# Kernel optimization log

Hardware: AMD Instinct MI355X
Metric: run time of the kernel (lower is better)

## Reference

```python
import jax, jax.numpy as jnp
import numpy as np

H_DIM = 64      # input_dim of edge_aggregation (== h_dim)
HID = 128       # hidden_size of each per-edge-type agg MLP
T = 5           # edge_types for non-nba dataset
B, E, N = 64, 1024, 512


def setup_inputs() -> dict:
    key = jax.random.key(0)
    ks = jax.random.split(key, 8)
    edge_distribution = jax.random.uniform(ks[0], (B, E, T), dtype=jnp.float32)
    H = jax.random.uniform(ks[1], (B, E, N), dtype=jnp.float32)
    ori = jax.random.normal(ks[2], (B, N, H_DIM), dtype=jnp.float32)
    s1 = 1.0 / np.sqrt(H_DIM)
    s2 = 1.0 / np.sqrt(HID)
    # stacked per-edge-type MLP params: Linear(64->128) -> ReLU -> Linear(128->64)
    W1 = jax.random.uniform(ks[3], (T, H_DIM, HID), minval=-s1, maxval=s1, dtype=jnp.float32)
    b1 = jax.random.uniform(ks[4], (T, HID), minval=-s1, maxval=s1, dtype=jnp.float32)
    W2 = jax.random.uniform(ks[5], (T, HID, H_DIM), minval=-s2, maxval=s2, dtype=jnp.float32)
    b2 = jax.random.uniform(ks[6], (T, H_DIM), minval=-s2, maxval=s2, dtype=jnp.float32)
    return {"edge_distribution": edge_distribution, "H": H, "ori": ori,
            "W1": W1, "b1": b1, "W2": W2, "b2": b2}


def reference(edge_distribution, H, ori, W1, b1, W2, b2):
    # incidence gather: hyperedge features [B, E, D]
    edges = jnp.matmul(H, ori)
    # per-edge-type 2-layer MLP, vectorized over the T edge types
    h = jax.nn.relu(jnp.einsum('bed,tdh->bteh', edges, W1) + b1[None, :, None, :])
    per_type = jnp.einsum('bteh,thd->bted', h, W2) + b2[None, :, None, :]
    # mixture-weighted sum over edge types -> [B, E, D]
    edge_feature = jnp.einsum('bet,bted->bed', edge_distribution, per_type)
    # scatter back through H^T and concat with original node features
    node_agg = jnp.einsum('ben,bed->bnd', H, edge_feature)  # H^T @ edge_feature
    node_feature = jnp.concatenate((node_agg, ori), axis=-1)  # [B, N, 2D]
    return node_feature
```

## Files before the change

### kernel.cpp

```cpp
#include <hip/hip_runtime.h>

#define B_   64
#define E_   1024
#define N_   512
#define D_   64
#define HID_ 128
#define T_   5

typedef __bf16 bf16x8 __attribute__((ext_vector_type(8)));
typedef float f32x4 __attribute__((ext_vector_type(4)));

__device__ __forceinline__ unsigned short f2bu(float f) {
    union { float f; unsigned int u; } v; v.f = f;
    unsigned int r = (v.u + 0x7fffu + ((v.u >> 16) & 1u)) >> 16;
    return (unsigned short)r;
}

__device__ __forceinline__ unsigned int pack2(float lo, float hi) {
    union { __bf16 b[2]; unsigned int u; } v;
    v.b[0] = (__bf16)lo; v.b[1] = (__bf16)hi;
    return v.u;
}

__device__ __forceinline__ uint4 cvt8(float4 a, float4 b) {
    union { __bf16 h[8]; uint4 u; } v;
    v.h[0] = (__bf16)a.x; v.h[1] = (__bf16)a.y; v.h[2] = (__bf16)a.z; v.h[3] = (__bf16)a.w;
    v.h[4] = (__bf16)b.x; v.h[5] = (__bf16)b.y; v.h[6] = (__bf16)b.z; v.h[7] = (__bf16)b.w;
    return v.u;
}

#define MFMA16(a, b, c) __builtin_amdgcn_mfma_f32_16x16x32_bf16((a), (b), (c), 0, 0, 0)

__global__ __launch_bounds__(256) void k_prep_w(const float* __restrict__ W1,
                                                const float* __restrict__ W2,
                                                unsigned short* __restrict__ W1T,
                                                unsigned short* __restrict__ W2T) {
    int idx = blockIdx.x * 256 + threadIdx.x;
    if (idx < T_ * HID_ * D_) {
        int t = idx / (HID_ * D_), rem = idx % (HID_ * D_);
        int h = rem / D_, d = rem % D_;
        W1T[idx] = f2bu(W1[(t * D_ + d) * HID_ + h]);
    } else {
        int j = idx - T_ * HID_ * D_;
        int t = j / (D_ * HID_), rem = j % (D_ * HID_);
        int d = rem / HID_, h = rem % HID_;
        W2T[j] = f2bu(W2[(t * HID_ + h) * D_ + d]);
    }
}

__global__ __launch_bounds__(256) void k_ori_prep(const float* __restrict__ ori,
                                                  float* __restrict__ out,
                                                  unsigned short* __restrict__ oriT) {
    int b = blockIdx.y, n0 = blockIdx.x * 64;
    __shared__ float tl[64 * 65];
    int tid = threadIdx.x;
    int dl = tid & 63;
    #pragma unroll 4
    for (int p = 0; p < 16; ++p) {
        int nn = p * 4 + (tid >> 6);
        float v = ori[(size_t)(b * N_ + n0 + nn) * D_ + dl];
        out[(size_t)(b * N_ + n0 + nn) * 128 + 64 + dl] = v;
        tl[dl * 65 + nn] = v;
    }
    __syncthreads();
    #pragma unroll 4
    for (int p = 0; p < 16; ++p) {
        int dd = p * 4 + (tid >> 6);
        oriT[(size_t)(b * D_ + dd) * N_ + n0 + dl] = f2bu(tl[dd * 65 + dl]);
    }
}

__global__ __launch_bounds__(256) void k_edge_mlp(const float* __restrict__ H,
                                                  const unsigned short* __restrict__ oriT,
                                                  const float* __restrict__ ed,
                                                  const float* __restrict__ b1,
                                                  const float* __restrict__ b2,
                                                  const unsigned short* __restrict__ W1T,
                                                  const unsigned short* __restrict__ W2T,
                                                  unsigned short* __restrict__ efT) {
    int bx = blockIdx.x;
    int b = bx >> 4, e0 = (bx & 15) * 64;
    __shared__ __align__(16) unsigned short X[17920];
    __shared__ __align__(16) unsigned short a_sh[64 * 72];
    __shared__ __align__(16) unsigned short h_sh[64 * 136];
    __shared__ float wd_sh[320];
    __shared__ float b1_sh[640];
    __shared__ float b2_sh[320];
    int tid = threadIdx.x, w = tid >> 6, l = tid & 63, q = l >> 4, c = l & 15;

    for (int u = tid; u < 320; u += 256) wd_sh[u] = ed[((size_t)b * E_ + e0) * T_ + u];
    for (int u = tid; u < 640; u += 256) b1_sh[u] = b1[u];
    for (int u = tid; u < 320; u += 256) b2_sh[u] = b2[u];

    const f32x4 zero = {0.f, 0.f, 0.f, 0.f};

    unsigned short* aA = X;
    unsigned short* bB = X + 4608;
    f32x4 acc1[4];
    #pragma unroll
    for (int fn = 0; fn < 4; ++fn) acc1[fn] = zero;

    for (int ks = 0; ks < 8; ++ks) {
        int k0 = ks * 64;
        #pragma unroll
        for (int p = 0; p < 2; ++p) {
            int u = p * 256 + tid, r = u >> 3, sg = u & 7;
            const float* s = &H[((size_t)b * E_ + e0 + r) * N_ + k0 + sg * 8];
            float4 f0 = *(const float4*)&s[0];
            float4 f1 = *(const float4*)&s[4];
            *(uint4*)&aA[r * 72 + sg * 8] = cvt8(f0, f1);
        }
        #pragma unroll
        for (int p = 0; p < 2; ++p) {
            int u = p * 256 + tid, r = u >> 3, sg = u & 7;
            *(uint4*)&bB[r * 72 + sg * 8] =
                *(const uint4*)&oriT[((size_t)b * D_ + r) * N_ + k0 + sg * 8];
        }
        __syncthreads();
        #pragma unroll
        for (int h = 0; h < 2; ++h) {
            bf16x8 a0 = *(const bf16x8*)&aA[(w * 16 + c) * 72 + h * 32 + q * 8];
            #pragma unroll
            for (int fn = 0; fn < 4; ++fn) {
                bf16x8 bb = *(const bf16x8*)&bB[(fn * 16 + c) * 72 + h * 32 + q * 8];
                acc1[fn] = MFMA16(a0, bb, acc1[fn]);
            }
        }
        __syncthreads();
    }

    #pragma unroll
    for (int fn = 0; fn < 4; ++fn)
        #pragma unroll
        for (int i = 0; i < 4; ++i)
            a_sh[(w * 16 + q * 4 + i) * 72 + fn * 16 + c] = f2bu(acc1[fn][i]);

    bf16x8 afr[2];
    #pragma unroll
    for (int ks = 0; ks < 2; ++ks)
        afr[ks] = *(const bf16x8*)&a_sh[(w * 16 + c) * 72 + ks * 32 + q * 8];

    unsigned short* w1_sh = X;
    unsigned short* w2_sh = X + 9216;

    f32x4 y[4];
    #pragma unroll
    for (int fn = 0; fn < 4; ++fn) y[fn] = zero;

    for (int t = 0; t < T_; ++t) {
        #pragma unroll
        for (int p = 0; p < 4; ++p) {
            int u2 = p * 256 + tid, hh = u2 >> 3, sg = u2 & 7;
            *(uint4*)&w1_sh[hh * 72 + sg * 8] =
                *(const uint4*)&W1T[((size_t)t * HID_ + hh) * D_ + sg * 8];
        }
        #pragma unroll
        for (int p = 0; p < 4; ++p) {
            int u2 = p * 256 + tid, dd = u2 >> 4, sg = u2 & 15;
            *(uint4*)&w2_sh[dd * 136 + sg * 8] =
                *(const uint4*)&W2T[((size_t)t * D_ + dd) * HID_ + sg * 8];
        }
        __syncthreads();

        f32x4 hc[8];
        #pragma unroll
        for (int fn = 0; fn < 8; ++fn) hc[fn] = zero;
        #pragma unroll
        for (int ks = 0; ks < 2; ++ks) {
            #pragma unroll
            for (int fn = 0; fn < 8; ++fn) {
                bf16x8 bb = *(const bf16x8*)&w1_sh[(fn * 16 + c) * 72 + ks * 32 + q * 8];
                hc[fn] = MFMA16(afr[ks], bb, hc[fn]);
            }
        }
        float wv[4];
        #pragma unroll
        for (int i = 0; i < 4; ++i) wv[i] = wd_sh[(w * 16 + q * 4 + i) * T_ + t];
        #pragma unroll
        for (int fn = 0; fn < 8; ++fn) {
            float b1v = b1_sh[t * HID_ + fn * 16 + c];
            #pragma unroll
            for (int i = 0; i < 4; ++i) {
                float v = hc[fn][i] + b1v;
                v = fmaxf(v, 0.0f) * wv[i];
                h_sh[(w * 16 + q * 4 + i) * 136 + fn * 16 + c] = f2bu(v);
            }
        }
        #pragma unroll
        for (int ks = 0; ks < 4; ++ks) {
            bf16x8 a = *(const bf16x8*)&h_sh[(w * 16 + c) * 136 + ks * 32 + q * 8];
            #pragma unroll
            for (int fn = 0; fn < 4; ++fn) {
                bf16x8 bb = *(const bf16x8*)&w2_sh[(fn * 16 + c) * 136 + ks * 32 + q * 8];
                y[fn] = MFMA16(a, bb, y[fn]);
            }
        }
        if (t < T_ - 1) __syncthreads();
    }

    #pragma unroll
    for (int fn = 0; fn < 4; ++fn) {
        int d = fn * 16 + c;
        ushort4 o;
        #pragma unroll
        for (int i = 0; i < 4; ++i) {
            int r = w * 16 + q * 4 + i;
            float s = y[fn][i];
            #pragma unroll
            for (int t = 0; t < T_; ++t) s += wd_sh[r * T_ + t] * b2_sh[t * D_ + d];
            ((unsigned short*)&o)[i] = f2bu(s);
        }
        *(ushort4*)&efT[((size_t)b * D_ + d) * E_ + e0 + w * 16 + q * 4] = o;
    }
}

__global__ __launch_bounds__(256) void k_gemm_out(const float* __restrict__ H,
                                                  const unsigned short* __restrict__ efT,
                                                  float* __restrict__ out) {
    int bid = blockIdx.x;
    int swz = (bid & 7) * 64 + (bid >> 3);
    int b = swz >> 3, n0 = (swz & 7) * 64;
    __shared__ __align__(16) unsigned short aA[2][64 * 72];
    __shared__ unsigned int bB32[2][64 * 33];
    int tid = threadIdx.x, w = tid >> 6, l = tid & 63, q = l >> 4, c = l & 15;
    int r2 = tid >> 3, cg = tid & 7;
    const f32x4 zero = {0.f, 0.f, 0.f, 0.f};
    f32x4 acc[4];
    #pragma unroll
    for (int fm = 0; fm < 4; ++fm) acc[fm] = zero;

    const unsigned short* Ab = &efT[(size_t)b * D_ * E_];
    const float* Hb = &H[(size_t)b * E_ * N_ + n0];

    uint4 ar0, ar1;
    float4 f0, f1, g0, g1;
    {
        ar0 = *(const uint4*)&Ab[(size_t)r2 * E_ + cg * 8];
        ar1 = *(const uint4*)&Ab[(size_t)(r2 + 32) * E_ + cg * 8];
        const float* s0 = Hb + (size_t)(2 * r2) * N_ + cg * 8;
        const float* s1 = s0 + N_;
        f0 = *(const float4*)&s0[0]; f1 = *(const float4*)&s0[4];
        g0 = *(const float4*)&s1[0]; g1 = *(const float4*)&s1[4];
    }
    {
        *(uint4*)&aA[0][r2 * 72 + cg * 8] = ar0;
        *(uint4*)&aA[0][(r2 + 32) * 72 + cg * 8] = ar1;
        float r0a[8] = {f0.x, f0.y, f0.z, f0.w, f1.x, f1.y, f1.z, f1.w};
        float r1a[8] = {g0.x, g0.y, g0.z, g0.w, g1.x, g1.y, g1.z, g1.w};
        #pragma unroll
        for (int j = 0; j < 8; ++j)
            bB32[0][(cg * 8 + j) * 33 + r2] = pack2(r0a[j], r1a[j]);
    }
    __syncthreads();

    for (int ks = 0; ks < 16; ++ks) {
        if (ks < 15) {
            int k0 = (ks + 1) * 64;
            ar0 = *(const uint4*)&Ab[(size_t)r2 * E_ + k0 + cg * 8];
            ar1 = *(const uint4*)&Ab[(size_t)(r2 + 32) * E_ + k0 + cg * 8];
            const float* s0 = Hb + (size_t)(k0 + 2 * r2) * N_ + cg * 8;
            const float* s1 = s0 + N_;
            f0 = *(const float4*)&s0[0]; f1 = *(const float4*)&s0[4];
            g0 = *(const float4*)&s1[0]; g1 = *(const float4*)&s1[4];
        }
        int cur = ks & 1;
        #pragma unroll
        for (int hh = 0; hh < 2; ++hh) {
            union { unsigned int u[4]; bf16x8 v; } bb;
            #pragma unroll
            for (int i = 0; i < 4; ++i)
                bb.u[i] = bB32[cur][(w * 16 + c) * 33 + hh * 16 + q * 4 + i];
            #pragma unroll
            for (int fm = 0; fm < 4; ++fm) {
                bf16x8 afr = *(const bf16x8*)&aA[cur][(fm * 16 + c) * 72 + hh * 32 + q * 8];
                acc[fm] = MFMA16(afr, bb.v, acc[fm]);
            }
        }
        if (ks < 15) {
            int nxt = cur ^ 1;
            *(uint4*)&aA[nxt][r2 * 72 + cg * 8] = ar0;
            *(uint4*)&aA[nxt][(r2 + 32) * 72 + cg * 8] = ar1;
            float r0a[8] = {f0.x, f0.y, f0.z, f0.w, f1.x, f1.y, f1.z, f1.w};
            float r1a[8] = {g0.x, g0.y, g0.z, g0.w, g1.x, g1.y, g1.z, g1.w};
            #pragma unroll
            for (int j = 0; j < 8; ++j)
                bB32[nxt][(cg * 8 + j) * 33 + r2] = pack2(r0a[j], r1a[j]);
            __syncthreads();
        }
    }
    #pragma unroll
    for (int fm = 0; fm < 4; ++fm) {
        *(f32x4*)&out[((size_t)b * N_ + n0 + w * 16 + c) * 128 + fm * 16 + q * 4] = acc[fm];
    }
}

extern "C" void kernel_launch(void* const* d_in, const int* in_sizes, int n_in,
                              void* d_out, int out_size, void* d_ws, size_t ws_size,
                              hipStream_t stream) {
    const float* ed  = (const float*)d_in[0];
    const float* H   = (const float*)d_in[1];
    const float* ori = (const float*)d_in[2];
    const float* W1  = (const float*)d_in[3];
    const float* b1  = (const float*)d_in[4];
    const float* W2  = (const float*)d_in[5];
    const float* b2  = (const float*)d_in[6];
    float* out = (float*)d_out;

    char* ws = (char*)d_ws;
    unsigned short* oriT = (unsigned short*)ws; ws += (size_t)B_ * D_ * N_ * 2;
    unsigned short* W1T  = (unsigned short*)ws; ws += (size_t)T_ * HID_ * D_ * 2;
    unsigned short* W2T  = (unsigned short*)ws; ws += (size_t)T_ * D_ * HID_ * 2;
    unsigned short* efT  = (unsigned short*)ws; ws += (size_t)B_ * D_ * E_ * 2;

    hipLaunchKernelGGL(k_prep_w, dim3(320), dim3(256), 0, stream, W1, W2, W1T, W2T);
    hipLaunchKernelGGL(k_ori_prep, dim3(8, 64), dim3(256), 0, stream, ori, out, oriT);
    hipLaunchKernelGGL(k_edge_mlp, dim3(1024), dim3(256), 0, stream,
                       H, oriT, ed, b1, b2, W1T, W2T, efT);
    hipLaunchKernelGGL(k_gemm_out, dim3(512), dim3(256), 0, stream, H, efT, out);
}
```

Before: 267.2 us.

## Split output GEMM over E into two halves with a reduce pass, shrink MLP LDS

The final H^T @ edge_feature GEMM is split along the E dimension into two halves. This doubles the grid to 1024 blocks for better occupancy across CUs. Each half writes fp32 partials to workspace, and a new reduce kernel sums them into the output. Separately, the edge MLP kernel now stages W1 and W2 through one shared buffer in turn, which cuts LDS use and may allow more resident blocks, at the cost of extra barriers and one more kernel launch plus partial-buffer traffic.

```diff
diff --git a/kernel.cpp b/kernel.cpp
--- a/kernel.cpp
+++ b/kernel.cpp
@@ -80,7 +80,7 @@
                                                   unsigned short* __restrict__ efT) {
     int bx = blockIdx.x;
     int b = bx >> 4, e0 = (bx & 15) * 64;
-    __shared__ __align__(16) unsigned short X[17920];
+    __shared__ __align__(16) unsigned short X[9216];
     __shared__ __align__(16) unsigned short a_sh[64 * 72];
     __shared__ __align__(16) unsigned short h_sh[64 * 136];
     __shared__ float wd_sh[320];
@@ -128,49 +128,36 @@
         }
         __syncthreads();
     }
-
     #pragma unroll
     for (int fn = 0; fn < 4; ++fn)
         #pragma unroll
         for (int i = 0; i < 4; ++i)
             a_sh[(w * 16 + q * 4 + i) * 72 + fn * 16 + c] = f2bu(acc1[fn][i]);
 
-    bf16x8 afr[2];
-    #pragma unroll
-    for (int ks = 0; ks < 2; ++ks)
-        afr[ks] = *(const bf16x8*)&a_sh[(w * 16 + c) * 72 + ks * 32 + q * 8];
-
-    unsigned short* w1_sh = X;
-    unsigned short* w2_sh = X + 9216;
-
+    unsigned short* w_sh = X;
     f32x4 y[4];
     #pragma unroll
     for (int fn = 0; fn < 4; ++fn) y[fn] = zero;
 
     for (int t = 0; t < T_; ++t) {
+        __syncthreads();
         #pragma unroll
         for (int p = 0; p < 4; ++p) {
-            int u2 = p * 256 + tid, hh = u2 >> 3, sg = u2 & 7;
-            *(uint4*)&w1_sh[hh * 72 + sg * 8] =
-                *(const uint4*)&W1T[((size_t)t * HID_ + hh) * D_ + sg * 8];
-        }
-        #pragma unroll
-        for (int p = 0; p < 4; ++p) {
-            int u2 = p * 256 + tid, dd = u2 >> 4, sg = u2 & 15;
-            *(uint4*)&w2_sh[dd * 136 + sg * 8] =
-                *(const uint4*)&W2T[((size_t)t * D_ + dd) * HID_ + sg * 8];
-        }
-        __syncthreads();
-
+            int u = p * 256 + tid, hh = u >> 3, sg = u & 7;
+            *(uint4*)&w_sh[hh * 72 + sg * 8] =
+                *(const uint4*)&W1T[(t * HID_ + hh) * D_ + sg * 8];
+        }
+        __syncthreads();
         f32x4 hc[8];
         #pragma unroll
         for (int fn = 0; fn < 8; ++fn) hc[fn] = zero;
         #pragma unroll
         for (int ks = 0; ks < 2; ++ks) {
+            bf16x8 a = *(const bf16x8*)&a_sh[(w * 16 + c) * 72 + ks * 32 + q * 8];
             #pragma unroll
             for (int fn = 0; fn < 8; ++fn) {
-                bf16x8 bb = *(const bf16x8*)&w1_sh[(fn * 16 + c) * 72 + ks * 32 + q * 8];
-                hc[fn] = MFMA16(afr[ks], bb, hc[fn]);
+                bf16x8 bb = *(const bf16x8*)&w_sh[(fn * 16 + c) * 72 + ks * 32 + q * 8];
+                hc[fn] = MFMA16(a, bb, hc[fn]);
             }
         }
         float wv[4];
@@ -186,18 +173,24 @@
                 h_sh[(w * 16 + q * 4 + i) * 136 + fn * 16 + c] = f2bu(v);
             }
         }
+        __syncthreads();
+        #pragma unroll
+        for (int p = 0; p < 4; ++p) {
+            int u = p * 256 + tid, dd = u >> 4, sg = u & 15;
+            *(uint4*)&w_sh[dd * 136 + sg * 8] =
+                *(const uint4*)&W2T[(t * D_ + dd) * HID_ + sg * 8];
+        }
+        __syncthreads();
         #pragma unroll
         for (int ks = 0; ks < 4; ++ks) {
             bf16x8 a = *(const bf16x8*)&h_sh[(w * 16 + c) * 136 + ks * 32 + q * 8];
             #pragma unroll
             for (int fn = 0; fn < 4; ++fn) {
-                bf16x8 bb = *(const bf16x8*)&w2_sh[(fn * 16 + c) * 136 + ks * 32 + q * 8];
+                bf16x8 bb = *(const bf16x8*)&w_sh[(fn * 16 + c) * 136 + ks * 32 + q * 8];
                 y[fn] = MFMA16(a, bb, y[fn]);
             }
         }
-        if (t < T_ - 1) __syncthreads();
-    }
-
+    }
     #pragma unroll
     for (int fn = 0; fn < 4; ++fn) {
         int d = fn * 16 + c;
@@ -216,10 +209,11 @@
 
 __global__ __launch_bounds__(256) void k_gemm_out(const float* __restrict__ H,
                                                   const unsigned short* __restrict__ efT,
-                                                  float* __restrict__ out) {
+                                                  float* __restrict__ partial) {
     int bid = blockIdx.x;
-    int swz = (bid & 7) * 64 + (bid >> 3);
-    int b = swz >> 3, n0 = (swz & 7) * 64;
+    int swz = (bid & 7) * 128 + (bid >> 3);
+    int b = swz >> 4, n0 = ((swz >> 1) & 7) * 64, kh = swz & 1;
+    int eb = kh * 512;
     __shared__ __align__(16) unsigned short aA[2][64 * 72];
     __shared__ unsigned int bB32[2][64 * 33];
     int tid = threadIdx.x, w = tid >> 6, l = tid & 63, q = l >> 4, c = l & 15;
@@ -229,8 +223,8 @@
     #pragma unroll
     for (int fm = 0; fm < 4; ++fm) acc[fm] = zero;
 
-    const unsigned short* Ab = &efT[(size_t)b * D_ * E_];
-    const float* Hb = &H[(size_t)b * E_ * N_ + n0];
+    const unsigned short* Ab = &efT[(size_t)b * D_ * E_ + eb];
+    const float* Hb = &H[((size_t)b * E_ + eb) * N_ + n0];
 
     uint4 ar0, ar1;
     float4 f0, f1, g0, g1;
@@ -253,15 +247,15 @@
     }
     __syncthreads();
 
-    for (int ks = 0; ks < 16; ++ks) {
-        if (ks < 15) {
+    for (int ks = 0; ks < 8; ++ks) {
+        if (ks < 7) {
             int k0 = (ks + 1) * 64;
             ar0 = *(const uint4*)&Ab[(size_t)r2 * E_ + k0 + cg * 8];
             ar1 = *(const uint4*)&Ab[(size_t)(r2 + 32) * E_ + k0 + cg * 8];
             const float* s0 = Hb + (size_t)(k0 + 2 * r2) * N_ + cg * 8;
             const float* s1 = s0 + N_;
             f0 = *(const float4*)&s0[0]; f1 = *(const float4*)&s0[4];
-            g0 = *(const float4*)&s1[0]; g1 = *(const float4*)&s1[4];
+        g0 = *(const float4*)&s1[0]; g1 = *(const float4*)&s1[4];
         }
         int cur = ks & 1;
         #pragma unroll
@@ -276,7 +270,7 @@
                 acc[fm] = MFMA16(afr, bb.v, acc[fm]);
             }
         }
-        if (ks < 15) {
+        if (ks < 7) {
             int nxt = cur ^ 1;
             *(uint4*)&aA[nxt][r2 * 72 + cg * 8] = ar0;
             *(uint4*)&aA[nxt][(r2 + 32) * 72 + cg * 8] = ar1;
@@ -288,10 +282,24 @@
             __syncthreads();
         }
     }
+    float* pp = &partial[(((size_t)kh * B_ + b) * N_ + n0 + w * 16 + c) * D_];
     #pragma unroll
     for (int fm = 0; fm < 4; ++fm) {
-        *(f32x4*)&out[((size_t)b * N_ + n0 + w * 16 + c) * 128 + fm * 16 + q * 4] = acc[fm];
-    }
+        *(f32x4*)&pp[fm * 16 + q * 4] = acc[fm];
+    }
+}
+
+__global__ __launch_bounds__(256) void k_reduce(const float* __restrict__ partial,
+                                                float* __restrict__ out) {
+    int gid = blockIdx.x * 256 + threadIdx.x;
+    int r = gid >> 4;
+    int dq = (gid & 15) * 4;
+    const float* p0 = &partial[(size_t)r * D_ + dq];
+    const float* p1 = p0 + (size_t)B_ * N_ * D_;
+    float4 a = *(const float4*)p0;
+    float4 bb = *(const float4*)p1;
+    float4 s = {a.x + bb.x, a.y + bb.y, a.z + bb.z, a.w + bb.w};
+    *(float4*)&out[(size_t)r * 128 + dq] = s;
 }
 
 extern "C" void kernel_launch(void* const* d_in, const int* in_sizes, int n_in,
@@ -307,14 +315,17 @@
     float* out = (float*)d_out;
 
     char* ws = (char*)d_ws;
-    unsigned short* oriT = (unsigned short*)ws; ws += (size_t)B_ * D_ * N_ * 2;
-    unsigned short* W1T  = (unsigned short*)ws; ws += (size_t)T_ * HID_ * D_ * 2;
-    unsigned short* W2T  = (unsigned short*)ws; ws += (size_t)T_ * D_ * HID_ * 2;
-    unsigned short* efT  = (unsigned short*)ws; ws += (size_t)B_ * D_ * E_ * 2;
+    size_t used = 0;
+    unsigned short* oriT = (unsigned short*)(ws + used); used += (size_t)B_ * D_ * N_ * 2;
+    unsigned short* W1T  = (unsigned short*)(ws + used); used += (size_t)T_ * HID_ * D_ * 2;
+    unsigned short* W2T  = (unsigned short*)(ws + used); used += (size_t)T_ * D_ * HID_ * 2;
+    unsigned short* efT  = (unsigned short*)(ws + used); used += (size_t)B_ * D_ * E_ * 2;
+    float* partial = (float*)(ws + used); used += (size_t)2 * B_ * N_ * D_ * 4;
 
     hipLaunchKernelGGL(k_prep_w, dim3(320), dim3(256), 0, stream, W1, W2, W1T, W2T);
     hipLaunchKernelGGL(k_ori_prep, dim3(8, 64), dim3(256), 0, stream, ori, out, oriT);
     hipLaunchKernelGGL(k_edge_mlp, dim3(1024), dim3(256), 0, stream,
                        H, oriT, ed, b1, b2, W1T, W2T, efT);
-    hipLaunchKernelGGL(k_gemm_out, dim3(512), dim3(256), 0, stream, H, efT, out);
-}
+    hipLaunchKernelGGL(k_gemm_out, dim3(1024), dim3(256), 0, stream, H, efT, partial);
+    hipLaunchKernelGGL(k_reduce, dim3(2048), dim3(256), 0, stream, partial, out);
+}
```

After: 284.1 us. +6.3%, slower.
